# Kernel optimization log

Measured on AMD Instinct MI355X. Metric: run time of the kernel, lower is better.

Reference implementation:

```python
import jax, jax.numpy as jnp
import numpy as np
from jax import lax

# pywt db4 filters. REC_LO is pywt's rec_lo; the others follow pywt's QMF relations:
# rec_hi[k] = (-1)**k * rec_lo[F-1-k]; dec_lo = rec_lo[::-1]; dec_hi = rec_hi[::-1].
REC_LO = np.array([0.23037781330885523, 0.7148465705525415, 0.6308807679295904,
                   -0.027983769416983849, -0.18703481171888114, 0.030841381835986965,
                   0.032883011666982945, -0.010597401784997278], dtype=np.float32)
F = 8
REC_HI = np.array([(-1.0) ** k * REC_LO[F - 1 - k] for k in range(F)], dtype=np.float32)
DEC_LO = REC_LO[::-1].copy()
DEC_HI = REC_HI[::-1].copy()
LEVELS = 3


def _conv(x, kern, stride=1, lhs_dilation=1, padding=((0, 0),)):
    # x: (N, 1, L) ; 1-D correlation (jax conv does NOT flip the kernel)
    k = jnp.asarray(kern, x.dtype).reshape(1, 1, -1)
    return lax.conv_general_dilated(x, k, window_strides=(stride,), padding=padding,
                                    lhs_dilation=(lhs_dilation,),
                                    dimension_numbers=('NCH', 'OIH', 'NCH'))


def dwt(x):
    # pywt single-level dwt, mode='symmetric': extend by F-1 each side, then
    # decimated convolution with dec filters. Equivalent to: drop first extended
    # sample and stride-2 correlate with reversed dec filter (= rec filter).
    xe = jnp.pad(x, ((0, 0), (0, 0), (F - 1, F - 1)), mode='symmetric')[..., 1:]
    cA = _conv(xe, REC_LO, stride=2)   # rev(DEC_LO) == REC_LO
    cD = _conv(xe, REC_HI, stride=2)   # rev(DEC_HI) == REC_HI
    return cA, cD


def idwt(a, d):
    # pywt idwt: upsample by 2 (zeros between samples, len 2L-1), full-convolve
    # with rec filters, trim F-2 from each side -> len 2L - F + 2.
    # Via dilated conv: lhs_dilation=2, pad 1 each side, correlate with rev(rec)=dec.
    ra = _conv(a, DEC_LO, lhs_dilation=2, padding=((1, 1),))
    rd = _conv(d, DEC_HI, lhs_dilation=2, padding=((1, 1),))
    return ra + rd


def waverec(coeffs):
    a = coeffs[0]
    for d in coeffs[1:]:
        if a.shape[-1] == d.shape[-1] + 1:
            a = a[..., :-1]
        a = idwt(a, d)
    return a


def setup_inputs() -> dict:
    key = jax.random.key(0)
    x = jax.random.normal(key, (32, 64, 8192), dtype=jnp.float32)
    return {"x": x}


def reference(x):
    B, C, n = x.shape
    a = x.reshape(B * C, 1, n)
    details = []
    for _ in range(LEVELS):
        a, d = dwt(a)
        details.append(d)
    coeffs = [a] + details[::-1]  # [cA_L, cD_L, ..., cD_1] as in pywt.wavedec
    bands = []
    for i in range(LEVELS + 1):
        kept = [c if j == i else jnp.zeros_like(c) for j, c in enumerate(coeffs)]
        rec = waverec(kept)[..., :n]
        bands.append(rec.reshape(B, C, n))
    return tuple(bands)
```

## Files before the change

kernel.cpp:

```cpp
#include <hip/hip_runtime.h>


#define T      256
#define N0     8192
#define L1     4099
#define L2     2053
#define L3     1030
#define NROWS  2048
#define TW     1024

#define RL0 0.23037781330885523f
#define RL1 0.7148465705525415f
#define RL2 0.6308807679295904f
#define RL3 (-0.02798376941698385f)
#define RL4 (-0.18703481171888114f)
#define RL5 0.030841381835986965f
#define RL6 0.032883011666982945f
#define RL7 (-0.010597401784997278f)

__device__ __forceinline__ int reflect(int m, int n)
{
    m = (m < 0) ? (-1 - m) : m;
    m = (m >= n) ? (2 * n - 1 - m) : m;
    return m;
}

__device__ __forceinline__ void fwd_win(const float* __restrict__ src, int src_lo,
                                        float* __restrict__ dstA, float* __restrict__ dstD,
                                        int out_lo, int out_len, int Lv, int tid)
{
    const float lo[8] = {RL0, RL1, RL2, RL3, RL4, RL5, RL6, RL7};
    const float hi[8] = {RL7, -RL6, RL5, -RL4, RL3, -RL2, RL1, -RL0};
    for (int idx = tid; idx < out_len; idx += T) {
        int g  = out_lo + idx;
        int ge = reflect(g, Lv);
        int b  = 2 * ge - 6 - src_lo;
        float sa = 0.f, sd = 0.f;
#pragma unroll
        for (int k = 0; k < 8; ++k) {
            float v = src[b + k];
            sa = fmaf(v, lo[k], sa);
            sd = fmaf(v, hi[k], sd);
        }
        dstA[idx] = sa;
        dstD[idx] = sd;
    }
}

__device__ __forceinline__ void up_win(const float* __restrict__ src, int src_lo,
                                       float* __restrict__ dst, int t0, int pairs,
                                       float o0, float o1, float o2, float o3,
                                       float e0, float e1, float e2, float e3, int tid)
{
    for (int idx = tid; idx < pairs; idx += T) {
        int b = t0 + idx - src_lo;
        float s0 = src[b], s1 = src[b + 1], s2 = src[b + 2], s3 = src[b + 3];
        float ev = s0 * e0 + s1 * e1 + s2 * e2 + s3 * e3;
        float od = s0 * o0 + s1 * o1 + s2 * o2 + s3 * o3;
        ((float2*)dst)[idx] = make_float2(ev, od);
    }
}

__device__ __forceinline__ void fin_win(const float* __restrict__ src, int src_lo, int n0,
                                        float* __restrict__ g,
                                        float o0, float o1, float o2, float o3,
                                        float e0, float e1, float e2, float e3, int tid)
{
    int b = (n0 >> 1) + 2 * tid - src_lo;
    float s0 = src[b], s1 = src[b + 1], s2 = src[b + 2], s3 = src[b + 3], s4 = src[b + 4];
    float4 o;
    o.x = s0 * e0 + s1 * e1 + s2 * e2 + s3 * e3;
    o.y = s0 * o0 + s1 * o1 + s2 * o2 + s3 * o3;
    o.z = s1 * e0 + s2 * e1 + s3 * e2 + s4 * e3;
    o.w = s1 * o0 + s2 * o1 + s3 * o2 + s4 * o3;
    ((float4*)(g + n0))[tid] = o;
}

#define POOL_F 3088

__global__ __launch_bounds__(T) void wavelet_bands(const float* __restrict__ x,
                                                   float* __restrict__ out)
{
    __shared__ float buf[POOL_F];
    const int tid  = threadIdx.x;
    const int bid  = blockIdx.x;
    const int row  = bid >> 3;
    const int tile = bid & 7;
    const int n0   = tile * TW;

    const int lo1 = (n0 >> 1) - 18;
    const int lo2 = (n0 >> 2) - 6;
    const int lo3 = (n0 >> 3);
    const int lox = n0 - 48;

    float* a1w = buf;
    float* d1w = buf + 560;
    float* a2w = buf + 1120;
    float* d2w = buf + 1400;
    float* a3w = buf + 1680;
    float* d3w = buf + 1816;
    float* xw  = buf + 1952;
    float* t2  = xw;
    float* t1a = xw + 520;
    float* t1d = xw + 784;
    float* t2d = buf;

    const float* xr = x + (size_t)row * N0;
    const size_t band = (size_t)NROWS * N0;
    float* o0p = out + (size_t)row * N0;
    float* o1p = o0p + band;
    float* o2p = o0p + 2 * band;
    float* o3p = o0p + 3 * band;

    for (int idx = tid; idx < 1128; idx += T)
        xw[idx] = xr[reflect(lox + idx, N0)];
    __syncthreads();

    fwd_win(xw, lox, a1w, d1w, lo1, 558, L1, tid);
    __syncthreads();

    fwd_win(a1w, lo1, a2w, d2w, lo2, 276, L2, tid);
    fin_win(d1w, lo1, n0, o3p, -RL0, -RL2, -RL4, -RL6, RL1, RL3, RL5, RL7, tid);
    __syncthreads();

    fwd_win(a2w, lo2, a3w, d3w, lo3, 135, L3, tid);
    up_win(d2w, lo2, t2, n0 >> 2, 258, -RL0, -RL2, -RL4, -RL6, RL1, RL3, RL5, RL7, tid);
    __syncthreads();

    fin_win(t2, n0 >> 1, n0, o2p, RL7, RL5, RL3, RL1, RL6, RL4, RL2, RL0, tid);
    up_win(a3w, lo3, t1a, n0 >> 3, 131, RL7, RL5, RL3, RL1, RL6, RL4, RL2, RL0, tid);
    up_win(d3w, lo3, t1d, n0 >> 3, 131, -RL0, -RL2, -RL4, -RL6, RL1, RL3, RL5, RL7, tid);
    __syncthreads();

    up_win(t1a, n0 >> 2, t2,  n0 >> 2, 258, RL7, RL5, RL3, RL1, RL6, RL4, RL2, RL0, tid);
    up_win(t1d, n0 >> 2, t2d, n0 >> 2, 258, RL7, RL5, RL3, RL1, RL6, RL4, RL2, RL0, tid);
    __syncthreads();

    fin_win(t2,  n0 >> 1, n0, o0p, RL7, RL5, RL3, RL1, RL6, RL4, RL2, RL0, tid);
    fin_win(t2d, n0 >> 1, n0, o1p, RL7, RL5, RL3, RL1, RL6, RL4, RL2, RL0, tid);
}

extern "C" void kernel_launch(void* const* d_in, const int* in_sizes, int n_in,
                              void* d_out, int out_size, void* d_ws, size_t ws_size,
                              hipStream_t stream)
{
    const float* x = (const float*)d_in[0];
    float* out = (float*)d_out;
    wavelet_bands<<<NROWS * 8, T, 0, stream>>>(x, out);
}
```

Measured before the change: 318.8 us.

## Split each block's tile into per-wavefront subtiles to drop block barriers

Each 64-lane wavefront now processes its own 256-sample tile end to end in a private shared-memory slice, so every __syncthreads between stages is removed and only wavefront-synchronous execution orders the stages. Interior tiles load input with float4 global reads, and the filter stages read shared memory as float2 pairs. The price is more halo recomputation per output, since 256-wide tiles carry the same fixed halos as before. Correctness also depends on lockstep execution within a wavefront with no explicit wave barrier, and on the float2/float4 loads being aligned.

```diff
diff --git a/kernel.cpp b/kernel.cpp
--- a/kernel.cpp
+++ b/kernel.cpp
@@ -7,7 +7,8 @@
 #define L2     2053
 #define L3     1030
 #define NROWS  2048
-#define TW     1024
+#define TW     256
+#define WSLICE 960
 
 #define RL0 0.23037781330885523f
 #define RL1 0.7148465705525415f
@@ -27,20 +28,22 @@
 
 __device__ __forceinline__ void fwd_win(const float* __restrict__ src, int src_lo,
                                         float* __restrict__ dstA, float* __restrict__ dstD,
-                                        int out_lo, int out_len, int Lv, int tid)
+                                        int out_lo, int out_len, int Lv, int lane)
 {
     const float lo[8] = {RL0, RL1, RL2, RL3, RL4, RL5, RL6, RL7};
     const float hi[8] = {RL7, -RL6, RL5, -RL4, RL3, -RL2, RL1, -RL0};
-    for (int idx = tid; idx < out_len; idx += T) {
+    const float2* s2 = (const float2*)src;
+    for (int idx = lane; idx < out_len; idx += 64) {
         int g  = out_lo + idx;
         int ge = reflect(g, Lv);
-        int b  = 2 * ge - 6 - src_lo;
+        int h  = (2 * ge - 6 - src_lo) >> 1;
+        float2 p0 = s2[h], p1 = s2[h + 1], p2 = s2[h + 2], p3 = s2[h + 3];
+        float w[8] = {p0.x, p0.y, p1.x, p1.y, p2.x, p2.y, p3.x, p3.y};
         float sa = 0.f, sd = 0.f;
 #pragma unroll
         for (int k = 0; k < 8; ++k) {
-            float v = src[b + k];
-            sa = fmaf(v, lo[k], sa);
-            sd = fmaf(v, hi[k], sd);
+            sa = fmaf(w[k], lo[k], sa);
+            sd = fmaf(w[k], hi[k], sd);
         }
         dstA[idx] = sa;
         dstD[idx] = sd;
@@ -50,9 +53,9 @@
 __device__ __forceinline__ void up_win(const float* __restrict__ src, int src_lo,
                                        float* __restrict__ dst, int t0, int pairs,
                                        float o0, float o1, float o2, float o3,
-                                       float e0, float e1, float e2, float e3, int tid)
+                                       float e0, float e1, float e2, float e3, int lane)
 {
-    for (int idx = tid; idx < pairs; idx += T) {
+    for (int idx = lane; idx < pairs; idx += 64) {
         int b = t0 + idx - src_lo;
         float s0 = src[b], s1 = src[b + 1], s2 = src[b + 2], s3 = src[b + 3];
         float ev = s0 * e0 + s1 * e1 + s2 * e2 + s3 * e3;
@@ -61,49 +64,54 @@
     }
 }
 
-__device__ __forceinline__ void fin_win(const float* __restrict__ src, int src_lo, int n0,
+__device__ __forceinline__ void fin_win(const float* __restrict__ src, int src_lo, int w0,
                                         float* __restrict__ g,
                                         float o0, float o1, float o2, float o3,
-                                        float e0, float e1, float e2, float e3, int tid)
+                                        float e0, float e1, float e2, float e3, int lane)
 {
-    int b = (n0 >> 1) + 2 * tid - src_lo;
-    float s0 = src[b], s1 = src[b + 1], s2 = src[b + 2], s3 = src[b + 3], s4 = src[b + 4];
+    int b = (w0 >> 1) + 2 * lane - src_lo;
+    const float2* s2 = (const float2*)src;
+    float2 q0 = s2[b >> 1], q1 = s2[(b >> 1) + 1];
+    float s4 = src[b + 4];
+    float a0 = q0.x, a1 = q0.y, a2 = q1.x, a3 = q1.y;
     float4 o;
-    o.x = s0 * e0 + s1 * e1 + s2 * e2 + s3 * e3;
-    o.y = s0 * o0 + s1 * o1 + s2 * o2 + s3 * o3;
-    o.z = s1 * e0 + s2 * e1 + s3 * e2 + s4 * e3;
-    o.w = s1 * o0 + s2 * o1 + s3 * o2 + s4 * o3;
-    ((float4*)(g + n0))[tid] = o;
+    o.x = a0 * e0 + a1 * e1 + a2 * e2 + a3 * e3;
+    o.y = a0 * o0 + a1 * o1 + a2 * o2 + a3 * o3;
+    o.z = a1 * e0 + a2 * e1 + a3 * e2 + s4 * e3;
+    o.w = a1 * o0 + a2 * o1 + a3 * o2 + s4 * o3;
+    ((float4*)(g + w0))[lane] = o;
 }
 
-#define POOL_F 3088
 
 __global__ __launch_bounds__(T) void wavelet_bands(const float* __restrict__ x,
                                                    float* __restrict__ out)
 {
-    __shared__ float buf[POOL_F];
+    __shared__ float buf[4 * WSLICE];
     const int tid  = threadIdx.x;
+    const int lane = tid & 63;
+    const int wid  = tid >> 6;
     const int bid  = blockIdx.x;
     const int row  = bid >> 3;
-    const int tile = bid & 7;
-    const int n0   = tile * TW;
+    const int w0   = ((bid & 7) * 4 + wid) * TW;
 
-    const int lo1 = (n0 >> 1) - 18;
-    const int lo2 = (n0 >> 2) - 6;
-    const int lo3 = (n0 >> 3);
-    const int lox = n0 - 48;
+    float* wbuf = buf + wid * WSLICE;
+    float* xw  = wbuf;
+    float* a1w = wbuf + 360;
+    float* d1w = wbuf + 534;
+    float* a2w = wbuf + 708;
+    float* d2w = wbuf + 792;
+    float* a3w = wbuf + 876;
+    float* d3w = wbuf + 915;
+    float* t2  = wbuf;
+    float* t1a = wbuf + 136;
+    float* t1d = wbuf + 208;
+    float* t2a = wbuf + 360;
+    float* t2d = wbuf + 534;
 
-    float* a1w = buf;
-    float* d1w = buf + 560;
-    float* a2w = buf + 1120;
-    float* d2w = buf + 1400;
-    float* a3w = buf + 1680;
-    float* d3w = buf + 1816;
-    float* xw  = buf + 1952;
-    float* t2  = xw;
-    float* t1a = xw + 520;
-    float* t1d = xw + 784;
-    float* t2d = buf;
+    const int lo1 = (w0 >> 1) - 18;
+    const int lo2 = (w0 >> 2) - 6;
+    const int lo3 = (w0 >> 3);
+    const int lox = w0 - 48;
 
     const float* xr = x + (size_t)row * N0;
     const size_t band = (size_t)NROWS * N0;
@@ -112,32 +120,34 @@
     float* o2p = o0p + 2 * band;
     float* o3p = o0p + 3 * band;
 
-    for (int idx = tid; idx < 1128; idx += T)
-        xw[idx] = xr[reflect(lox + idx, N0)];
-    __syncthreads();
+    if (w0 == 0 || w0 == N0 - TW) {
+        for (int idx = lane; idx < 360; idx += 64)
+            xw[idx] = xr[reflect(lox + idx, N0)];
+    } else {
+        const float4* xr4 = (const float4*)xr;
+        float4* xw4 = (float4*)xw;
+        const int q0 = lox >> 2;
+        for (int i = lane; i < 90; i += 64)
+            xw4[i] = xr4[q0 + i];
+    }
 
-    fwd_win(xw, lox, a1w, d1w, lo1, 558, L1, tid);
-    __syncthreads();
+    fwd_win(xw, lox, a1w, d1w, lo1, TW / 2 + 46, L1, lane);
 
-    fwd_win(a1w, lo1, a2w, d2w, lo2, 276, L2, tid);
-    fin_win(d1w, lo1, n0, o3p, -RL0, -RL2, -RL4, -RL6, RL1, RL3, RL5, RL7, tid);
-    __syncthreads();
+    fwd_win(a1w, lo1, a2w, d2w, lo2, TW / 4 + 20, L2, lane);
+    fin_win(d1w, lo1, w0, o3p, -RL0, -RL2, -RL4, -RL6, RL1, RL3, RL5, RL7, lane);
 
-    fwd_win(a2w, lo2, a3w, d3w, lo3, 135, L3, tid);
-    up_win(d2w, lo2, t2, n0 >> 2, 258, -RL0, -RL2, -RL4, -RL6, RL1, RL3, RL5, RL7, tid);
-    __syncthreads();
+    fwd_win(a2w, lo2, a3w, d3w, lo3, TW / 8 + 7, L3, lane);
+    up_win(d2w, lo2, t2, w0 >> 2, TW / 4 + 2, -RL0, -RL2, -RL4, -RL6, RL1, RL3, RL5, RL7, lane);
 
-    fin_win(t2, n0 >> 1, n0, o2p, RL7, RL5, RL3, RL1, RL6, RL4, RL2, RL0, tid);
-    up_win(a3w, lo3, t1a, n0 >> 3, 131, RL7, RL5, RL3, RL1, RL6, RL4, RL2, RL0, tid);
-    up_win(d3w, lo3, t1d, n0 >> 3, 131, -RL0, -RL2, -RL4, -RL6, RL1, RL3, RL5, RL7, tid);
-    __syncthreads();
+    fin_win(t2, w0 >> 1, w0, o2p, RL7, RL5, RL3, RL1, RL6, RL4, RL2, RL0, lane);
+    up_win(a3w, lo3, t1a, w0 >> 3, TW / 8 + 3, RL7, RL5, RL3, RL1, RL6, RL4, RL2, RL0, lane);
+    up_win(d3w, lo3, t1d, w0 >> 3, TW / 8 + 3, -RL0, -RL2, -RL4, -RL6, RL1, RL3, RL5, RL7, lane);
 
-    up_win(t1a, n0 >> 2, t2,  n0 >> 2, 258, RL7, RL5, RL3, RL1, RL6, RL4, RL2, RL0, tid);
-    up_win(t1d, n0 >> 2, t2d, n0 >> 2, 258, RL7, RL5, RL3, RL1, RL6, RL4, RL2, RL0, tid);
-    __syncthreads();
+    up_win(t1a, w0 >> 2, t2a, w0 >> 2, TW / 4 + 2, RL7, RL5, RL3, RL1, RL6, RL4, RL2, RL0, lane);
+    up_win(t1d, w0 >> 2, t2d, w0 >> 2, TW / 4 + 2, RL7, RL5, RL3, RL1, RL6, RL4, RL2, RL0, lane);
 
-    fin_win(t2,  n0 >> 1, n0, o0p, RL7, RL5, RL3, RL1, RL6, RL4, RL2, RL0, tid);
-    fin_win(t2d, n0 >> 1, n0, o1p, RL7, RL5, RL3, RL1, RL6, RL4, RL2, RL0, tid);
+    fin_win(t2a, w0 >> 1, w0, o0p, RL7, RL5, RL3, RL1, RL6, RL4, RL2, RL0, lane);
+    fin_win(t2d, w0 >> 1, w0, o1p, RL7, RL5, RL3, RL1, RL6, RL4, RL2, RL0, lane);
 }
 
 extern "C" void kernel_launch(void* const* d_in, const int* in_sizes, int n_in,
```

Result: no change. 313.9 us, median of 2 (-1.5%).
